# Kernel tuning notes

Measured on AMD Instinct MI355X. Metric: run time of the kernel, lower is better.

## Reference

```python
import jax, jax.numpy as jnp
import numpy as np


def setup_inputs() -> dict:
    key = jax.random.key(0)
    ks = jax.random.split(key, 7)
    b, c, t, h, w = 4, 128, 16, 64, 64
    c8 = c // 8
    return {
        "x": jax.random.normal(ks[0], (b, c, t, h, w), dtype=jnp.float32),
        "q_w": jax.random.normal(ks[1], (c8, c), dtype=jnp.float32) * 0.05,
        "q_b": jax.random.normal(ks[2], (c8,), dtype=jnp.float32) * 0.05,
        "k_w": jax.random.normal(ks[3], (c8, c), dtype=jnp.float32) * 0.05,
        "k_b": jax.random.normal(ks[4], (c8,), dtype=jnp.float32) * 0.05,
        "v_w": jax.random.normal(ks[5], (c, c), dtype=jnp.float32) * 0.05,
        "v_b": jax.random.normal(ks[6], (c,), dtype=jnp.float32) * 0.05,
        "gamma": jnp.zeros((1,), dtype=jnp.float32),
    }


def reference(x, q_w, q_b, k_w, k_b, v_w, v_b, gamma):
    # x: [b, c, t, h, w]. 1x1x1 Conv3d == per-position channel matmul.
    # Project directly into the [b, h, w, t, ch] layout the attention uses.
    q = jnp.einsum('bcthw,oc->bhwto', x, q_w) + q_b   # [b,h,w,t,c/8]
    k = jnp.einsum('bcthw,oc->bhwto', x, k_w) + k_b   # [b,h,w,t,c/8]
    v = jnp.einsum('bcthw,oc->bhwto', x, v_w) + v_b   # [b,h,w,t,c]
    # Temporal attention batched over (b,h,w): scores [b,h,w,t_q,t_k]
    scores = jnp.einsum('bhwio,bhwjo->bhwij', q, k)
    attn = jax.nn.softmax(scores, axis=-1)            # softmax over keys (dim=2 in torch [bhw,t,t])
    out = jnp.einsum('bhwij,bhwjo->bhwio', attn, v)   # [b,h,w,t,c]
    out = jnp.transpose(out, (0, 4, 3, 1, 2))         # -> [b,c,t,h,w]
    return gamma * out + x
```

## Files before the change

### kernel.cpp

```cpp
#include <hip/hip_runtime.h>


#define C_  128
#define T_  16
#define H_  64
#define W_  64
#define CO_ 160
#define WT_ 16
#define NBLK 1024
#define THW (T_*H_*W_)

typedef float  f32x4  __attribute__((ext_vector_type(4)));
typedef short  bf16x4 __attribute__((ext_vector_type(4)));
typedef short  bf16x8 __attribute__((ext_vector_type(8)));

__device__ __forceinline__ unsigned short f2bf(float f) {
    union { float f; unsigned u; } v; v.f = f;
    unsigned r = v.u + 0x7fffu + ((v.u >> 16) & 1u);
    return (unsigned short)(r >> 16);
}
__device__ __forceinline__ float bf2f(unsigned short s) {
    union { unsigned u; float f; } v; v.u = ((unsigned)s) << 16;
    return v.f;
}

__global__ __launch_bounds__(256) void tsa_prepack(
        const float* __restrict__ qw, const float* __restrict__ qb,
        const float* __restrict__ kw, const float* __restrict__ kb,
        const float* __restrict__ vw, const float* __restrict__ vb,
        unsigned short* __restrict__ W2, float* __restrict__ b2) {
    int i = blockIdx.x * 256 + threadIdx.x;
    int o = i >> 7, c = i & 127;
    float v = (o < 16) ? qw[o * C_ + c] : (o < 32) ? kw[(o - 16) * C_ + c]
                                                   : vw[(o - 32) * C_ + c];
    W2[i] = f2bf(v);
    if (i < CO_) b2[i] = (i < 16) ? qb[i] : (i < 32) ? kb[i - 16] : vb[i - 32];
}

#define PS 2184
#define TS 136
#define IDX_X(pos, t, c)      ((pos) * PS + (t) * TS + (c))
#define IDX_QK(pos, qk, t, o) (((((pos) * 2 + (qk)) * T_ + (t)) * 16) + (o))
#define OS_W 132
#define OS_T 2116
#define IDX_O(t, w, c)        ((t) * OS_T + (w) * OS_W + (c))
#define BUF_SH (T_ * PS)

__global__ __launch_bounds__(512, 4) void tsa_main(
        const float* __restrict__ x, const unsigned short* __restrict__ W2,
        const float* __restrict__ b2, const float* __restrict__ gamma,
        float* __restrict__ y) {

    __shared__ __align__(16) unsigned short buf[BUF_SH];

    int bid  = blockIdx.x;
    int work = (bid & 7) * (NBLK / 8) + (bid >> 3);
    int bh = work >> 2;
    int wt = work & 3;
    int b  = bh >> 6, h = bh & 63;
    int w0 = wt * WT_;

    const size_t base = (size_t)b * C_ * THW + (size_t)h * W_ + w0;
    const float* xb = x + base;
    float*       yb = y + base;

    const int tid = threadIdx.x;
    const int wq  = tid & 3;
    const int cs  = tid >> 2;
    const float g = gamma[0];

    {
        const float* xcol = xb + (size_t)cs * THW + wq * 4;
        f32x4 pb = *(const f32x4*)(xcol);
        #pragma unroll
        for (int t = 0; t < T_; ++t) {
            f32x4 cur = pb;
            if (t + 1 < T_) pb = *(const f32x4*)(xcol + (t + 1) * (H_ * W_));
            #pragma unroll
            for (int e = 0; e < 4; ++e)
                buf[IDX_X(wq * 4 + e, t, cs)] = f2bf(cur[e]);
        }
    }

    const int wv  = tid >> 6;
    const int lr  = tid & 15;
    const int grp = (tid & 63) >> 4;

    float biasv[10];
    #pragma unroll
    for (int nt = 0; nt < 10; ++nt) biasv[nt] = b2[nt * 16 + lr];

    __syncthreads();

    bf16x8 afrag[2][4];
    #pragma unroll
    for (int p = 0; p < 2; ++p)
        #pragma unroll
        for (int ks = 0; ks < 4; ++ks)
            afrag[p][ks] = *(const bf16x8*)&buf[IDX_X(wv * 2 + p, lr, ks * 32 + grp * 8)];

    __syncthreads();

    bf16x4 vreg[2][8];
    #pragma unroll
    for (int nt = 0; nt < 10; ++nt) {
        f32x4 acc0 = (f32x4){0.f, 0.f, 0.f, 0.f};
        f32x4 acc1 = (f32x4){0.f, 0.f, 0.f, 0.f};
        #pragma unroll
        for (int ks = 0; ks < 4; ++ks) {
            bf16x8 wf = *(const bf16x8*)&W2[(nt * 16 + lr) * C_ + ks * 32 + grp * 8];
            acc0 = __builtin_amdgcn_mfma_f32_16x16x32_bf16(afrag[0][ks], wf, acc0, 0, 0, 0);
            acc1 = __builtin_amdgcn_mfma_f32_16x16x32_bf16(afrag[1][ks], wf, acc1, 0, 0, 0);
        }
        if (nt < 2) {
            #pragma unroll
            for (int r = 0; r < 4; ++r) {
                buf[IDX_QK(wv * 2 + 0, nt, grp * 4 + r, lr)] = f2bf(acc0[r] + biasv[nt]);
                buf[IDX_QK(wv * 2 + 1, nt, grp * 4 + r, lr)] = f2bf(acc1[r] + biasv[nt]);
            }
        } else {
            bf16x4 p0, p1;
            #pragma unroll
            for (int r = 0; r < 4; ++r) {
                p0[r] = (short)f2bf(acc0[r] + biasv[nt]);
                p1[r] = (short)f2bf(acc1[r] + biasv[nt]);
            }
            vreg[0][nt - 2] = p0;
            vreg[1][nt - 2] = p1;
        }
    }
    __syncthreads();

    bf16x4 obf[2][8];
    #pragma unroll
    for (int p = 0; p < 2; ++p) {
        int pos = wv * 2 + p;
        bf16x4 kf = *(const bf16x4*)&buf[IDX_QK(pos, 1, lr, grp * 4)];
        bf16x4 qf = *(const bf16x4*)&buf[IDX_QK(pos, 0, lr, grp * 4)];
        f32x4 s = (f32x4){0.f, 0.f, 0.f, 0.f};
        s = __builtin_amdgcn_mfma_f32_16x16x16bf16_1k(kf, qf, s, 0, 0, 0);
        float mx = fmaxf(fmaxf(s[0], s[1]), fmaxf(s[2], s[3]));
        mx = fmaxf(mx, __shfl_xor(mx, 16));
        mx = fmaxf(mx, __shfl_xor(mx, 32));
        float e0 = __expf(s[0] - mx), e1 = __expf(s[1] - mx);
        float e2 = __expf(s[2] - mx), e3 = __expf(s[3] - mx);
        float sm = e0 + e1 + e2 + e3;
        sm += __shfl_xor(sm, 16);
        sm += __shfl_xor(sm, 32);
        float inv = 1.0f / sm;
        bf16x4 pf;
        pf[0] = (short)f2bf(e0 * inv); pf[1] = (short)f2bf(e1 * inv);
        pf[2] = (short)f2bf(e2 * inv); pf[3] = (short)f2bf(e3 * inv);
        #pragma unroll
        for (int ct = 0; ct < 8; ++ct) {
            f32x4 z = (f32x4){0.f, 0.f, 0.f, 0.f};
            z = __builtin_amdgcn_mfma_f32_16x16x16bf16_1k(vreg[p][ct], pf, z, 0, 0, 0);
            bf16x4 ob;
            #pragma unroll
            for (int r = 0; r < 4; ++r) ob[r] = (short)f2bf(z[r]);
            obf[p][ct] = ob;
        }
    }
    __syncthreads();

    #pragma unroll
    for (int p = 0; p < 2; ++p)
        #pragma unroll
        for (int ct = 0; ct < 8; ++ct)
            *(bf16x4*)&buf[IDX_O(lr, wv * 2 + p, ct * 16 + grp * 4)] = obf[p][ct];
    __syncthreads();

    {
        const float* xrow = xb + (size_t)cs * THW + wq * 4;
        float*       yrow = yb + (size_t)cs * THW + wq * 4;
        f32x4 pb = *(const f32x4*)(xrow);
        #pragma unroll
        for (int t = 0; t < T_; ++t) {
            f32x4 xv = pb;
            if (t + 1 < T_) pb = *(const f32x4*)(xrow + (t + 1) * (H_ * W_));
            f32x4 rv;
            #pragma unroll
            for (int e = 0; e < 4; ++e)
                rv[e] = fmaf(g, bf2f(buf[IDX_O(t, wq * 4 + e, cs)]), xv[e]);
            *(f32x4*)(yrow + t * (H_ * W_)) = rv;
        }
    }
}

extern "C" void kernel_launch(void* const* d_in, const int* in_sizes, int n_in,
                              void* d_out, int out_size, void* d_ws, size_t ws_size,
                              hipStream_t stream) {
    const float* x  = (const float*)d_in[0];
    const float* qw = (const float*)d_in[1];
    const float* qb = (const float*)d_in[2];
    const float* kw = (const float*)d_in[3];
    const float* kb = (const float*)d_in[4];
    const float* vw = (const float*)d_in[5];
    const float* vb = (const float*)d_in[6];
    const float* gm = (const float*)d_in[7];
    float* y = (float*)d_out;

    unsigned short* W2 = (unsigned short*)d_ws;
    float* b2 = (float*)((char*)d_ws + CO_ * C_ * sizeof(unsigned short));

    tsa_prepack<<<80, 256, 0, stream>>>(qw, qb, kw, kb, vw, vb, W2, b2);
    tsa_main<<<NBLK, 512, 0, stream>>>(x, W2, b2, gm, y);
}
```

Measured before the change: 104.6 us.

## Halve width tile, keep x in registers as bf16 for residual

The width tile shrinks from 16 to 8 positions, doubling the block count and halving the threads per block and the shared buffer. Each thread now issues all 16 time-step loads of x up front and keeps a bf16 copy in registers, so the final residual add no longer rereads x from global memory. This cuts global read traffic by roughly a third. In exchange the residual is added from bf16-rounded x instead of full fp32 x, which changes output precision (with gamma zero, the output becomes bf16-rounded x). It also raises register pressure.

```diff
diff --git a/kernel.cpp b/kernel.cpp
--- a/kernel.cpp
+++ b/kernel.cpp
@@ -5,9 +5,10 @@
 #define T_  16
 #define H_  64
 #define W_  64
+#define HW_ (H_*W_)
 #define CO_ 160
-#define WT_ 16
-#define NBLK 1024
+#define WT_ 8
+#define NBLK 2048
 #define THW (T_*H_*W_)
 
 typedef float  f32x4  __attribute__((ext_vector_type(4)));
@@ -41,12 +42,12 @@
 #define TS 136
 #define IDX_X(pos, t, c)      ((pos) * PS + (t) * TS + (c))
 #define IDX_QK(pos, qk, t, o) (((((pos) * 2 + (qk)) * T_ + (t)) * 16) + (o))
-#define OS_W 132
-#define OS_T 2116
+#define OS_W 136
+#define OS_T 1096
 #define IDX_O(t, w, c)        ((t) * OS_T + (w) * OS_W + (c))
-#define BUF_SH (T_ * PS)
-
-__global__ __launch_bounds__(512, 4) void tsa_main(
+#define BUF_SH 17536
+
+__global__ __launch_bounds__(256, 4) void tsa_main(
         const float* __restrict__ x, const unsigned short* __restrict__ W2,
         const float* __restrict__ b2, const float* __restrict__ gamma,
         float* __restrict__ y) {
@@ -55,8 +56,8 @@
 
     int bid  = blockIdx.x;
     int work = (bid & 7) * (NBLK / 8) + (bid >> 3);
-    int bh = work >> 2;
-    int wt = work & 3;
+    int bh = work >> 3;
+    int wt = work & 7;
     int b  = bh >> 6, h = bh & 63;
     int w0 = wt * WT_;
 
@@ -65,20 +66,35 @@
     float*       yb = y + base;
 
     const int tid = threadIdx.x;
-    const int wq  = tid & 3;
-    const int cs  = tid >> 2;
+    const int seg = tid & 1;
+    const int cs  = tid >> 1;
     const float g = gamma[0];
 
+    bf16x4 res[16];
     {
-        const float* xcol = xb + (size_t)cs * THW + wq * 4;
-        f32x4 pb = *(const f32x4*)(xcol);
-        #pragma unroll
-        for (int t = 0; t < T_; ++t) {
-            f32x4 cur = pb;
-            if (t + 1 < T_) pb = *(const f32x4*)(xcol + (t + 1) * (H_ * W_));
-            #pragma unroll
-            for (int e = 0; e < 4; ++e)
-                buf[IDX_X(wq * 4 + e, t, cs)] = f2bf(cur[e]);
+        const float* xcol = xb + (size_t)cs * THW + seg * 4;
+        f32x4 xrA[8], xrB[8];
+        #pragma unroll
+        for (int t = 0; t < 8; ++t) xrA[t] = *(const f32x4*)(xcol + t * HW_);
+        #pragma unroll
+        for (int t = 0; t < 8; ++t) xrB[t] = *(const f32x4*)(xcol + (t + 8) * HW_);
+        #pragma unroll
+        for (int t = 0; t < 8; ++t) {
+            #pragma unroll
+            for (int e = 0; e < 4; ++e) {
+                unsigned short u = f2bf(xrA[t][e]);
+                res[t][e] = (short)u;
+                buf[IDX_X(seg * 4 + e, t, cs)] = u;
+            }
+        }
+        #pragma unroll
+        for (int t = 0; t < 8; ++t) {
+            #pragma unroll
+            for (int e = 0; e < 4; ++e) {
+                unsigned short u = f2bf(xrB[t][e]);
+                res[t + 8][e] = (short)u;
+                buf[IDX_X(seg * 4 + e, t + 8, cs)] = u;
+            }
         }
     }
 
@@ -171,18 +187,15 @@
     __syncthreads();
 
     {
-        const float* xrow = xb + (size_t)cs * THW + wq * 4;
-        float*       yrow = yb + (size_t)cs * THW + wq * 4;
-        f32x4 pb = *(const f32x4*)(xrow);
+        float* yrow = yb + (size_t)cs * THW + seg * 4;
         #pragma unroll
         for (int t = 0; t < T_; ++t) {
-            f32x4 xv = pb;
-            if (t + 1 < T_) pb = *(const f32x4*)(xrow + (t + 1) * (H_ * W_));
             f32x4 rv;
             #pragma unroll
             for (int e = 0; e < 4; ++e)
-                rv[e] = fmaf(g, bf2f(buf[IDX_O(t, wq * 4 + e, cs)]), xv[e]);
-            *(f32x4*)(yrow + t * (H_ * W_)) = rv;
+                rv[e] = fmaf(g, bf2f(buf[IDX_O(t, seg * 4 + e, cs)]),
+                             bf2f((unsigned short)res[t][e]));
+            *(f32x4*)(yrow + t * HW_) = rv;
         }
     }
 }
@@ -204,5 +217,5 @@
     float* b2 = (float*)((char*)d_ws + CO_ * C_ * sizeof(unsigned short));
 
     tsa_prepack<<<80, 256, 0, stream>>>(qw, qb, kw, kb, vw, vb, W2, b2);
-    tsa_main<<<NBLK, 512, 0, stream>>>(x, W2, b2, gm, y);
-}
+    tsa_main<<<NBLK, 256, 0, stream>>>(x, W2, b2, gm, y);
+}
```

After: 162.2 us. 55.1% more time.

## Make blocks persistent over four W tiles with 1024 threads and prefetch next tile

Applied to the files above, without the earlier changes.

Each block now owns a whole (b,h) row and loops over four 16-wide W tiles using 1024 threads, one wavefront per position. While the current tile's projections run, it loads the next tile of x from global memory and stages it into a separate LDS region, overlapping loads with compute. The change also splits LDS into separate x, QK and output regions, so the shared buffer grows. The cost is fewer blocks (256), larger per-block LDS, lower occupancy, and more barriers per block.

```diff
diff --git a/kernel.cpp b/kernel.cpp
--- a/kernel.cpp
+++ b/kernel.cpp
@@ -5,9 +5,11 @@
 #define T_  16
 #define H_  64
 #define W_  64
+#define HW_ (H_*W_)
 #define CO_ 160
 #define WT_ 16
-#define NBLK 1024
+#define NTILE 4
+#define NBLK 256
 #define THW (T_*H_*W_)
 
 typedef float  f32x4  __attribute__((ext_vector_type(4)));
@@ -40,13 +42,15 @@
 #define PS 2184
 #define TS 136
 #define IDX_X(pos, t, c)      ((pos) * PS + (t) * TS + (c))
-#define IDX_QK(pos, qk, t, o) (((((pos) * 2 + (qk)) * T_ + (t)) * 16) + (o))
+#define QK_OFF 34944
+#define IDX_QK(pos, qk, t, o) (QK_OFF + ((((pos) * 2 + (qk)) * T_ + (t)) * 16) + (o))
+#define OUT_OFF 43136
 #define OS_W 132
 #define OS_T 2116
-#define IDX_O(t, w, c)        ((t) * OS_T + (w) * OS_W + (c))
-#define BUF_SH (T_ * PS)
-
-__global__ __launch_bounds__(512, 4) void tsa_main(
+#define IDX_O(t, w, c)        (OUT_OFF + (t) * OS_T + (w) * OS_W + (c))
+#define BUF_SH 76992
+
+__global__ __launch_bounds__(1024) void tsa_main(
         const float* __restrict__ x, const unsigned short* __restrict__ W2,
         const float* __restrict__ b2, const float* __restrict__ gamma,
         float* __restrict__ y) {
@@ -55,32 +59,17 @@
 
     int bid  = blockIdx.x;
     int work = (bid & 7) * (NBLK / 8) + (bid >> 3);
-    int bh = work >> 2;
-    int wt = work & 3;
-    int b  = bh >> 6, h = bh & 63;
-    int w0 = wt * WT_;
-
-    const size_t base = (size_t)b * C_ * THW + (size_t)h * W_ + w0;
+    int b  = work >> 6, h = work & 63;
+
+    const size_t base = (size_t)b * C_ * THW + (size_t)h * W_;
     const float* xb = x + base;
     float*       yb = y + base;
 
     const int tid = threadIdx.x;
-    const int wq  = tid & 3;
-    const int cs  = tid >> 2;
+    const int seg = tid & 3;
+    const int cs  = (tid >> 2) & 127;
+    const int hf  = tid >> 9;
     const float g = gamma[0];
-
-    {
-        const float* xcol = xb + (size_t)cs * THW + wq * 4;
-        f32x4 pb = *(const f32x4*)(xcol);
-        #pragma unroll
-        for (int t = 0; t < T_; ++t) {
-            f32x4 cur = pb;
-            if (t + 1 < T_) pb = *(const f32x4*)(xcol + (t + 1) * (H_ * W_));
-            #pragma unroll
-            for (int e = 0; e < 4; ++e)
-                buf[IDX_X(wq * 4 + e, t, cs)] = f2bf(cur[e]);
-        }
-    }
 
     const int wv  = tid >> 6;
     const int lr  = tid & 15;
@@ -90,99 +79,117 @@
     #pragma unroll
     for (int nt = 0; nt < 10; ++nt) biasv[nt] = b2[nt * 16 + lr];
 
-    __syncthreads();
-
-    bf16x8 afrag[2][4];
-    #pragma unroll
-    for (int p = 0; p < 2; ++p)
-        #pragma unroll
-        for (int ks = 0; ks < 4; ++ks)
-            afrag[p][ks] = *(const bf16x8*)&buf[IDX_X(wv * 2 + p, lr, ks * 32 + grp * 8)];
-
-    __syncthreads();
-
-    bf16x4 vreg[2][8];
-    #pragma unroll
-    for (int nt = 0; nt < 10; ++nt) {
-        f32x4 acc0 = (f32x4){0.f, 0.f, 0.f, 0.f};
-        f32x4 acc1 = (f32x4){0.f, 0.f, 0.f, 0.f};
-        #pragma unroll
-        for (int ks = 0; ks < 4; ++ks) {
-            bf16x8 wf = *(const bf16x8*)&W2[(nt * 16 + lr) * C_ + ks * 32 + grp * 8];
-            acc0 = __builtin_amdgcn_mfma_f32_16x16x32_bf16(afrag[0][ks], wf, acc0, 0, 0, 0);
-            acc1 = __builtin_amdgcn_mfma_f32_16x16x32_bf16(afrag[1][ks], wf, acc1, 0, 0, 0);
-        }
-        if (nt < 2) {
-            #pragma unroll
-            for (int r = 0; r < 4; ++r) {
-                buf[IDX_QK(wv * 2 + 0, nt, grp * 4 + r, lr)] = f2bf(acc0[r] + biasv[nt]);
-                buf[IDX_QK(wv * 2 + 1, nt, grp * 4 + r, lr)] = f2bf(acc1[r] + biasv[nt]);
-            }
-        } else {
-            bf16x4 p0, p1;
-            #pragma unroll
-            for (int r = 0; r < 4; ++r) {
-                p0[r] = (short)f2bf(acc0[r] + biasv[nt]);
-                p1[r] = (short)f2bf(acc1[r] + biasv[nt]);
-            }
-            vreg[0][nt - 2] = p0;
-            vreg[1][nt - 2] = p1;
-        }
+    {
+        const float* xc = xb + (size_t)cs * THW + seg * 4 + hf * 8 * HW_;
+        f32x4 xp[8];
+        #pragma unroll
+        for (int tt = 0; tt < 8; ++tt) xp[tt] = *(const f32x4*)(xc + tt * HW_);
+        #pragma unroll
+        for (int tt = 0; tt < 8; ++tt)
+            #pragma unroll
+            for (int e = 0; e < 4; ++e)
+                buf[IDX_X(seg * 4 + e, hf * 8 + tt, cs)] = f2bf(xp[tt][e]);
     }
     __syncthreads();
 
-    bf16x4 obf[2][8];
-    #pragma unroll
-    for (int p = 0; p < 2; ++p) {
-        int pos = wv * 2 + p;
-        bf16x4 kf = *(const bf16x4*)&buf[IDX_QK(pos, 1, lr, grp * 4)];
-        bf16x4 qf = *(const bf16x4*)&buf[IDX_QK(pos, 0, lr, grp * 4)];
-        f32x4 s = (f32x4){0.f, 0.f, 0.f, 0.f};
-        s = __builtin_amdgcn_mfma_f32_16x16x16bf16_1k(kf, qf, s, 0, 0, 0);
-        float mx = fmaxf(fmaxf(s[0], s[1]), fmaxf(s[2], s[3]));
-        mx = fmaxf(mx, __shfl_xor(mx, 16));
-        mx = fmaxf(mx, __shfl_xor(mx, 32));
-        float e0 = __expf(s[0] - mx), e1 = __expf(s[1] - mx);
-        float e2 = __expf(s[2] - mx), e3 = __expf(s[3] - mx);
-        float sm = e0 + e1 + e2 + e3;
-        sm += __shfl_xor(sm, 16);
-        sm += __shfl_xor(sm, 32);
-        float inv = 1.0f / sm;
-        bf16x4 pf;
-        pf[0] = (short)f2bf(e0 * inv); pf[1] = (short)f2bf(e1 * inv);
-        pf[2] = (short)f2bf(e2 * inv); pf[3] = (short)f2bf(e3 * inv);
-        #pragma unroll
-        for (int ct = 0; ct < 8; ++ct) {
-            f32x4 z = (f32x4){0.f, 0.f, 0.f, 0.f};
-            z = __builtin_amdgcn_mfma_f32_16x16x16bf16_1k(vreg[p][ct], pf, z, 0, 0, 0);
-            bf16x4 ob;
-            #pragma unroll
-            for (int r = 0; r < 4; ++r) ob[r] = (short)f2bf(z[r]);
-            obf[p][ct] = ob;
-        }
-    }
-    __syncthreads();
-
-    #pragma unroll
-    for (int p = 0; p < 2; ++p)
+    for (int i = 0; i < NTILE; ++i) {
+        const int w0 = i * WT_;
+
+        bf16x8 afrag[4];
+        #pragma unroll
+        for (int ks = 0; ks < 4; ++ks)
+            afrag[ks] = *(const bf16x8*)&buf[IDX_X(wv, lr, ks * 32 + grp * 8)];
+        __syncthreads();
+
+        f32x4 xn[8];
+        if (i + 1 < NTILE) {
+            const float* xc = xb + (w0 + WT_) + (size_t)cs * THW + seg * 4 + hf * 8 * HW_;
+            #pragma unroll
+            for (int tt = 0; tt < 8; ++tt) xn[tt] = *(const f32x4*)(xc + tt * HW_);
+        }
+
+        bf16x4 vreg[8];
+        #pragma unroll
+        for (int nt = 0; nt < 10; ++nt) {
+            f32x4 acc = (f32x4){0.f, 0.f, 0.f, 0.f};
+            #pragma unroll
+            for (int ks = 0; ks < 4; ++ks) {
+                bf16x8 wf = *(const bf16x8*)&W2[(nt * 16 + lr) * C_ + ks * 32 + grp * 8];
+                acc = __builtin_amdgcn_mfma_f32_16x16x32_bf16(afrag[ks], wf, acc, 0, 0, 0);
+            }
+            if (nt < 2) {
+                #pragma unroll
+                for (int r = 0; r < 4; ++r)
+                    buf[IDX_QK(wv, nt, grp * 4 + r, lr)] = f2bf(acc[r] + biasv[nt]);
+            } else {
+                bf16x4 pk;
+                #pragma unroll
+                for (int r = 0; r < 4; ++r) pk[r] = (short)f2bf(acc[r] + biasv[nt]);
+                vreg[nt - 2] = pk;
+            }
+        }
+
+        if (i + 1 < NTILE) {
+            #pragma unroll
+            for (int tt = 0; tt < 8; ++tt)
+                #pragma unroll
+                for (int e = 0; e < 4; ++e)
+                    buf[IDX_X(seg * 4 + e, hf * 8 + tt, cs)] = f2bf(xn[tt][e]);
+        }
+        __syncthreads();
+
+        bf16x4 obf[8];
+        {
+            bf16x4 kf = *(const bf16x4*)&buf[IDX_QK(wv, 1, lr, grp * 4)];
+            bf16x4 qf = *(const bf16x4*)&buf[IDX_QK(wv, 0, lr, grp * 4)];
+            f32x4 s = (f32x4){0.f, 0.f, 0.f, 0.f};
+            s = __builtin_amdgcn_mfma_f32_16x16x16bf16_1k(kf, qf, s, 0, 0, 0);
+            float mx = fmaxf(fmaxf(s[0], s[1]), fmaxf(s[2], s[3]));
+            mx = fmaxf(mx, __shfl_xor(mx, 16));
+            mx = fmaxf(mx, __shfl_xor(mx, 32));
+            float e0 = __expf(s[0] - mx), e1 = __expf(s[1] - mx);
+            float e2 = __expf(s[2] - mx), e3 = __expf(s[3] - mx);
+            float sm = e0 + e1 + e2 + e3;
+            sm += __shfl_xor(sm, 16);
+            sm += __shfl_xor(sm, 32);
+            float inv = 1.0f / sm;
+            bf16x4 pf;
+            pf[0] = (short)f2bf(e0 * inv); pf[1] = (short)f2bf(e1 * inv);
+            pf[2] = (short)f2bf(e2 * inv); pf[3] = (short)f2bf(e3 * inv);
+            #pragma unroll
+            for (int ct = 0; ct < 8; ++ct) {
+                f32x4 z = (f32x4){0.f, 0.f, 0.f, 0.f};
+                z = __builtin_amdgcn_mfma_f32_16x16x16bf16_1k(vreg[ct], pf, z, 0, 0, 0);
+                bf16x4 ob;
+                #pragma unroll
+                for (int r = 0; r < 4; ++r) ob[r] = (short)f2bf(z[r]);
+                obf[ct] = ob;
+            }
+        }
+
+        f32x4 xr[8];
+        {
+            const float* xc = xb + w0 + (size_t)cs * THW + seg * 4 + hf * 8 * HW_;
+            #pragma unroll
+            for (int tt = 0; tt < 8; ++tt) xr[tt] = *(const f32x4*)(xc + tt * HW_);
+        }
+
         #pragma unroll
         for (int ct = 0; ct < 8; ++ct)
-            *(bf16x4*)&buf[IDX_O(lr, wv * 2 + p, ct * 16 + grp * 4)] = obf[p][ct];
-    __syncthreads();
-
-    {
-        const float* xrow = xb + (size_t)cs * THW + wq * 4;
-        float*       yrow = yb + (size_t)cs * THW + wq * 4;
-        f32x4 pb = *(const f32x4*)(xrow);
-        #pragma unroll
-        for (int t = 0; t < T_; ++t) {
-            f32x4 xv = pb;
-            if (t + 1 < T_) pb = *(const f32x4*)(xrow + (t + 1) * (H_ * W_));
-            f32x4 rv;
-            #pragma unroll
-            for (int e = 0; e < 4; ++e)
-                rv[e] = fmaf(g, bf2f(buf[IDX_O(t, wq * 4 + e, cs)]), xv[e]);
-            *(f32x4*)(yrow + t * (H_ * W_)) = rv;
+            *(bf16x4*)&buf[IDX_O(lr, wv, ct * 16 + grp * 4)] = obf[ct];
+        __syncthreads();
+
+        {
+            float* yr = yb + w0 + (size_t)cs * THW + seg * 4 + hf * 8 * HW_;
+            #pragma unroll
+            for (int tt = 0; tt < 8; ++tt) {
+                int t = hf * 8 + tt;
+                f32x4 rv;
+                #pragma unroll
+                for (int e = 0; e < 4; ++e)
+                    rv[e] = fmaf(g, bf2f(buf[IDX_O(t, seg * 4 + e, cs)]), xr[tt][e]);
+                *(f32x4*)(yr + tt * HW_) = rv;
+            }
         }
     }
 }
@@ -204,5 +211,5 @@
     float* b2 = (float*)((char*)d_ws + CO_ * C_ * sizeof(unsigned short));
 
     tsa_prepack<<<80, 256, 0, stream>>>(qw, qb, kw, kb, vw, vb, W2, b2);
-    tsa_main<<<NBLK, 512, 0, stream>>>(x, W2, b2, gm, y);
-}
+    tsa_main<<<NBLK, 1024, 0, stream>>>(x, W2, b2, gm, y);
+}
```

After: 317.3 us. 3.03x slower.
